# Performance work log

Hardware: AMD Instinct MI355X
Metric: run time of the kernel (lower is better)

Reference implementation:

```python
import jax, jax.numpy as jnp
import numpy as np

B, S, E, H = 4, 2048, 1024, 16
D = E // H


def setup_inputs() -> dict:
    key = jax.random.key(0)
    ks = jax.random.split(key, 6)
    scale = 1.0 / np.sqrt(E).astype(np.float32)
    return {
        "x": jax.random.normal(ks[0], (B, S, E), jnp.float32),
        # positive entries -> cumsum normalizer is well conditioned
        "weight": jax.random.uniform(ks[1], (H, S), jnp.float32, 0.05, 1.0),
        "bias": jax.random.normal(ks[2], (H, S), jnp.float32) * 0.02,
        "inp_w": jax.random.normal(ks[3], (E, E), jnp.float32) * scale,
        "inp_b": jax.random.normal(ks[4], (E,), jnp.float32) * 0.02,
        "out_w": jax.random.normal(ks[5], (E, E), jnp.float32) * scale,
    }


def reference(x, weight, bias, inp_w, inp_b, out_w):
    Bx, Sx, Ex = x.shape
    Hx = weight.shape[0]
    Dx = Ex // Hx
    # input projection (torch Linear: x @ W.T + b)
    x = x @ inp_w.T + inp_b
    # (B,S,E) -> (B,E,S) -> (B,H,D,S)
    xh = x.transpose(0, 2, 1).reshape(Bx, Hx, Dx, Sx)
    # Toeplitz causal matrix per head: M[h,i,j] = weight[h, j-i] if j>=i else 0
    idx = jnp.arange(Sx)
    off = idx[None, :] - idx[:, None]  # (S,S)
    M = jnp.where(off >= 0, weight[:, off], jnp.zeros((), x.dtype))  # (H,S,S)
    # batched matmul over the sequence axis: y[b,h,d,t] = sum_s x[b,h,d,s] M[h,s,t]
    y = jnp.einsum('bhds,hst->bhdt', xh, M)
    # cumulative-sum normalization (do_toep_mean=True)
    norm = jnp.cumsum(weight, axis=-1)  # (H,S)
    y = y / norm[None, :, None, :]
    # per-head, per-position bias
    y = y + bias[None, :, None, :]
    # (B,H,D,S) -> (B,E,S) -> (B,S,E)
    y = y.reshape(Bx, Ex, Sx).transpose(0, 2, 1)
    # output projection (no bias)
    return y @ out_w.T
```

## Files before the change

### kernel.cpp

```cpp
#include <hip/hip_runtime.h>

typedef unsigned short u16;
typedef __attribute__((ext_vector_type(4))) float f32x4;
typedef __attribute__((ext_vector_type(8))) __bf16 bf16x8;

__device__ __forceinline__ u16 f2bf(float f) {
  unsigned u = __builtin_bit_cast(unsigned, f);
  u = u + 0x7fffu + ((u >> 16) & 1u);
  return (u16)(u >> 16);
}

__device__ __forceinline__ void load_lds16(const void* g, void* l) {
  __builtin_amdgcn_global_load_lds((__attribute__((address_space(1))) void*)g,
                                   (__attribute__((address_space(3))) void*)l,
                                   16, 0, 0);
}

__device__ __forceinline__ f32x4 MF(bf16x8 a, bf16x8 b, f32x4 c) {
  return __builtin_amdgcn_mfma_f32_16x16x32_bf16(a, b, c, 0, 0, 0);
}

__global__ __launch_bounds__(256) void prep_all(const float* __restrict__ x,
                                                const float* __restrict__ inp_w,
                                                const float* __restrict__ out_w,
                                                const float* __restrict__ weight,
                                                u16* __restrict__ Xb,
                                                u16* __restrict__ Wb,
                                                u16* __restrict__ OWb,
                                                float* __restrict__ normB,
                                                u16* __restrict__ V) {
  const int bx = blockIdx.x, tid = threadIdx.x;
  if (bx < 10240) {
    const float* src; u16* dst; int i;
    if (bx < 8192)      { src = x;     dst = Xb;  i = bx * 256 + tid; }
    else if (bx < 9216) { src = inp_w; dst = Wb;  i = (bx - 8192) * 256 + tid; }
    else                { src = out_w; dst = OWb; i = (bx - 9216) * 256 + tid; }
    const float4 v = ((const float4*)src)[i];
    ushort4 o;
    o.x = f2bf(v.x); o.y = f2bf(v.y); o.z = f2bf(v.z); o.w = f2bf(v.w);
    ((ushort4*)dst)[i] = o;
    return;
  }
  if (bx < 10256) {
    const int h = bx - 10240;
    __shared__ float ts[256];
    float v[8];
    const float* src = weight + h * 2048 + tid * 8;
    float s = 0.f;
#pragma unroll
    for (int j = 0; j < 8; ++j) v[j] = src[j];
#pragma unroll
    for (int j = 0; j < 8; ++j) { s += v[j]; v[j] = s; }
    ts[tid] = s;
    __syncthreads();
    float xx = s;
#pragma unroll
    for (int d = 1; d < 256; d <<= 1) {
      float y = (tid >= d) ? ts[tid - d] : 0.f;
      __syncthreads();
      xx += y;
      ts[tid] = xx;
      __syncthreads();
    }
    const float excl = xx - s;
    float* dst = normB + h * 2048 + tid * 8;
#pragma unroll
    for (int j = 0; j < 8; ++j) dst[j] = excl + v[j];
    return;
  }
  {
    const int bb = bx - 10256;
    const int h = bb & 15, tb = bb >> 4;
    __shared__ u16 wl[2048];
#pragma unroll
    for (int j = 0; j < 8; ++j) wl[tid * 8 + j] = f2bf(weight[h * 2048 + tid * 8 + j]);
    __syncthreads();
#pragma unroll
    for (int i = 0; i < 8; ++i) {
      const int cid = i * 256 + tid;
      const int row = cid >> 4, c = cid & 15;
      const int t = tb * 128 + row;
      const int j0 = c * 8;
      unsigned v[8];
#pragma unroll
      for (int jj = 0; jj < 8; ++jj) {
        const int j = j0 + jj;
        v[jj] = (t >= j) ? (unsigned)wl[t - j] : 0u;
      }
      uint4 o;
      o.x = v[0] | (v[1] << 16); o.y = v[2] | (v[3] << 16);
      o.z = v[4] | (v[5] << 16); o.w = v[6] | (v[7] << 16);
      *(uint4*)(V + ((size_t)(h * 2048 + t)) * 128 + j0) = o;
    }
  }
}

template <bool BIAS, bool F32OUT, int DEC>
__global__ __launch_bounds__(256) void gemm_nt4(const u16* __restrict__ A,
                                                const u16* __restrict__ B,
                                                void* __restrict__ C,
                                                const float* __restrict__ bias,
                                                int K, int lda, int ldb, int ldc) {
  __shared__ __align__(16) u16 As[2][128 * 64];
  __shared__ __align__(16) u16 Bs[2][128 * 64];
  const int tid = threadIdx.x;
  const int lane = tid & 63, wv = tid >> 6;
  const int wm = wv >> 1, wn = wv & 1;
  const int l15 = lane & 15, g = lane >> 4;

  const int flat = (int)blockIdx.x;
  int m0, n0;
  if (DEC == 0) {
    const int xcd = flat & 7, i = flat >> 3;
    m0 = (i & 7) * 128;
    n0 = ((xcd << 3) + (i >> 3)) * 128;
  } else {
    const int sw = (flat & 7) * 64 + (flat >> 3);
    m0 = (sw >> 3) * 128;
    n0 = (sw & 7) * 128;
  }

  const int NT = K >> 6;

  auto stage = [&](int t, int bi) {
    const int kt = t << 6;
#pragma unroll
    for (int i = 0; i < 4; ++i) {
      const int c = i * 256 + tid;
      const int row = c >> 3, cc = c & 7;
      load_lds16(A + (size_t)(m0 + row) * lda + kt + ((cc ^ (row & 7)) << 3),
                 &As[bi][i * 2048 + wv * 512]);
    }
#pragma unroll
    for (int i = 0; i < 4; ++i) {
      const int c = i * 256 + tid;
      const int row = c >> 3, cc = c & 7;
      load_lds16(B + (size_t)(n0 + row) * ldb + kt + ((cc ^ (row & 7)) << 3),
                 &Bs[bi][i * 2048 + wv * 512]);
    }
  };

  f32x4 acc[4][4] = {};
  stage(0, 0);
  __syncthreads();
  int cur = 0;
  for (int t = 0; t < NT; ++t) {
    if (t + 1 < NT) stage(t + 1, cur ^ 1);
#pragma unroll
    for (int kh = 0; kh < 2; ++kh) {
      bf16x8 af[4], bf[4];
#pragma unroll
      for (int mf = 0; mf < 4; ++mf) {
        const int row = wm * 64 + mf * 16 + l15;
        af[mf] = *(const bf16x8*)(&As[cur][row * 64 + ((((kh << 2) + g) ^ (row & 7)) << 3)]);
      }
#pragma unroll
      for (int nf = 0; nf < 4; ++nf) {
        const int row = wn * 64 + nf * 16 + l15;
        bf[nf] = *(const bf16x8*)(&Bs[cur][row * 64 + ((((kh << 2) + g) ^ (row & 7)) << 3)]);
      }
      __builtin_amdgcn_s_setprio(1);
#pragma unroll
      for (int mf = 0; mf < 4; ++mf)
#pragma unroll
        for (int nf = 0; nf < 4; ++nf)
          acc[mf][nf] = MF(af[mf], bf[nf], acc[mf][nf]);
      __builtin_amdgcn_s_setprio(0);
    }
    __syncthreads();
    cur ^= 1;
  }

#pragma unroll
  for (int mf = 0; mf < 4; ++mf) {
#pragma unroll
    for (int r = 0; r < 4; ++r) {
      const int row = m0 + wm * 64 + mf * 16 + g * 4 + r;
      const float bb = BIAS ? bias[row] : 0.f;
#pragma unroll
      for (int nf = 0; nf < 4; ++nf) {
        const int col = n0 + wn * 64 + nf * 16 + l15;
        const float v = acc[mf][nf][r] + bb;
        if (F32OUT)
          ((float*)C)[(size_t)row * ldc + col] = v;
        else
          ((u16*)C)[(size_t)row * ldc + col] = f2bf(v);
      }
    }
  }
}

__global__ __launch_bounds__(256) void toep_conv(const u16* __restrict__ X1t,
                                                 const u16* __restrict__ V,
                                                 const float* __restrict__ normB,
                                                 const float* __restrict__ biasB,
                                                 u16* __restrict__ Y2b) {
  __shared__ __align__(16) u16 As[3][128 * 64];
  __shared__ __align__(16) u16 Xs[3][64 * 64];
  const int tid = threadIdx.x;
  const int lane = tid & 63, wv = tid >> 6;
  const int l15 = lane & 15, g = lane >> 4;

  const int x = (int)blockIdx.x;
  const int h = (x & 7) + 8 * ((x >> 3) & 1);
  const int pb = x >> 4;
  const int pair = pb & 7, b = pb >> 3;

  const u16* Vh = V + (size_t)h * 2048 * 128;
  const u16* Xrow = X1t + (size_t)h * 64 * 8192 + b * 2048;

#pragma unroll 1
  for (int ti = 0; ti < 2; ++ti) {
    const int tt = ti ? pair : 15 - pair;
    const int t0 = tt * 128;
    const int Q = (tt + 1) * 2;
    f32x4 acc[2][4] = {};

    auto stage = [&](int q, int bufi) {
      const int st = q >> 1, k = q & 1;
      const u16* Ab = Vh + (size_t)(tt - st) * 128 * 128 + k * 64;
#pragma unroll
      for (int i = 0; i < 4; ++i) {
        const int c = i * 256 + tid;
        const int row = c >> 3, cc = c & 7;
        load_lds16(Ab + row * 128 + ((cc ^ (row & 7)) * 8),
                   &As[bufi][i * 2048 + wv * 512]);
      }
      const int s0 = st * 128 + k * 64;
#pragma unroll
      for (int i = 0; i < 2; ++i) {
        const int c = i * 256 + tid;
        const int row = c >> 3, cc = c & 7;
        load_lds16(Xrow + (size_t)row * 8192 + s0 + ((cc ^ (row & 7)) * 8),
                   &Xs[bufi][i * 2048 + wv * 512]);
      }
    };

    stage(0, 0);
    if (Q > 1) stage(1, 1);
    asm volatile("s_waitcnt vmcnt(6)" ::: "memory");
    __builtin_amdgcn_sched_barrier(0);
    __builtin_amdgcn_s_barrier();
    asm volatile("" ::: "memory");

    int cur = 0;
    for (int q = 0; q < Q; ++q) {
      if (q + 2 < Q) stage(q + 2, (q + 2) % 3);
#pragma unroll
      for (int ks = 0; ks < 2; ++ks) {
        bf16x8 af[2];
#pragma unroll
        for (int tf = 0; tf < 2; ++tf) {
          const int row = wv * 32 + tf * 16 + l15;
          af[tf] = *(const bf16x8*)(&As[cur][row * 64 + (((ks * 4 + g) ^ (row & 7)) * 8)]);
        }
#pragma unroll
        for (int nf = 0; nf < 4; ++nf) {
          const int row = nf * 16 + l15;
          const bf16x8 bv = *(const bf16x8*)(&Xs[cur][row * 64 + (((ks * 4 + g) ^ (row & 7)) * 8)]);
#pragma unroll
          for (int tf = 0; tf < 2; ++tf)
            acc[tf][nf] = MF(af[tf], bv, acc[tf][nf]);
        }
      }
      if (q + 2 < Q)      asm volatile("s_waitcnt vmcnt(6)" ::: "memory");
      else if (q + 1 < Q) asm volatile("s_waitcnt vmcnt(0)" ::: "memory");
      __builtin_amdgcn_sched_barrier(0);
      __builtin_amdgcn_s_barrier();
      asm volatile("" ::: "memory");
      cur = (cur == 2) ? 0 : cur + 1;
    }

#pragma unroll
    for (int tf = 0; tf < 2; ++tf) {
#pragma unroll
      for (int r = 0; r < 4; ++r) {
        const int t = t0 + wv * 32 + tf * 16 + g * 4 + r;
        const float inv = 1.0f / normB[h * 2048 + t];
        const float bb = biasB[h * 2048 + t];
#pragma unroll
        for (int nf = 0; nf < 4; ++nf) {
          const int d = nf * 16 + l15;
          Y2b[(size_t)(b * 2048 + t) * 1024 + h * 64 + d] = f2bf(acc[tf][nf][r] * inv + bb);
        }
      }
    }
  }
}

extern "C" void kernel_launch(void* const* d_in, const int* in_sizes, int n_in,
                              void* d_out, int out_size, void* d_ws, size_t ws_size,
                              hipStream_t stream) {
  (void)in_sizes; (void)n_in; (void)out_size; (void)ws_size;
  const float* x      = (const float*)d_in[0];
  const float* weight = (const float*)d_in[1];
  const float* biasB  = (const float*)d_in[2];
  const float* inp_w  = (const float*)d_in[3];
  const float* inp_b  = (const float*)d_in[4];
  const float* out_w  = (const float*)d_in[5];

  char* ws = (char*)d_ws;
  u16* Xb    = (u16*)(ws + 0);
  u16* X1t   = (u16*)(ws + (size_t)(16u << 20));
  u16* Y2b   = (u16*)(ws + (size_t)(32u << 20));
  u16* Wb    = (u16*)(ws + (size_t)(48u << 20));
  u16* OWb   = (u16*)(ws + (size_t)(50u << 20));
  float* normB = (float*)(ws + (size_t)(53u << 20));
  u16* Vt    = (u16*)(ws + (size_t)(56u << 20));

  prep_all<<<10512, 256, 0, stream>>>(x, inp_w, out_w, weight, Xb, Wb, OWb, normB, Vt);

  gemm_nt4<true, false, 0><<<512, 256, 0, stream>>>(
      Wb, Xb, (void*)X1t, inp_b, 1024, 1024, 1024, 8192);

  toep_conv<<<512, 256, 0, stream>>>(X1t, Vt, normB, biasB, Y2b);

  gemm_nt4<false, true, 1><<<512, 256, 0, stream>>>(
      Y2b, OWb, d_out, nullptr, 1024, 1024, 1024, 1024);
}
```

Measured before the change: 97.51 us.

## Share Toeplitz tile across two batches per block, double-buffer instead of triple

Each block of the Toeplitz convolution kernel now handles one output time tile for two batch elements at once, so each loaded Toeplitz (V) tile feeds twice as many MFMAs. The old scheme paired a short and a long time tile within one block. The new one maps short/long tiles across blocks through the v bit. The LDS pipeline drops from triple buffering with explicit vmcnt waits to double buffering with __syncthreads, and s_setprio is raised around the MFMA section. This doubles accumulator registers, may lose load balance, and may expose more memory latency than the deeper pipeline did.

```diff
diff --git a/kernel.cpp b/kernel.cpp
--- a/kernel.cpp
+++ b/kernel.cpp
@@ -195,93 +195,94 @@
                                                  const float* __restrict__ normB,
                                                  const float* __restrict__ biasB,
                                                  u16* __restrict__ Y2b) {
-  __shared__ __align__(16) u16 As[3][128 * 64];
-  __shared__ __align__(16) u16 Xs[3][64 * 64];
+  __shared__ __align__(16) u16 As[2][128 * 64];
+  __shared__ __align__(16) u16 Xs[2][2][64 * 64];
   const int tid = threadIdx.x;
   const int lane = tid & 63, wv = tid >> 6;
   const int l15 = lane & 15, g = lane >> 4;
 
   const int x = (int)blockIdx.x;
   const int h = (x & 7) + 8 * ((x >> 3) & 1);
-  const int pb = x >> 4;
-  const int pair = pb & 7, b = pb >> 3;
+  const int u = (x >> 4) & 15;
+  const int v = (x >> 8) & 1;
+  const int tt = v ? 15 - u : u;
+  const int t0 = tt * 128;
+  const int Q = (tt + 1) * 2;
 
   const u16* Vh = V + (size_t)h * 2048 * 128;
-  const u16* Xrow = X1t + (size_t)h * 64 * 8192 + b * 2048;
-
-#pragma unroll 1
-  for (int ti = 0; ti < 2; ++ti) {
-    const int tt = ti ? pair : 15 - pair;
-    const int t0 = tt * 128;
-    const int Q = (tt + 1) * 2;
-    f32x4 acc[2][4] = {};
-
-    auto stage = [&](int q, int bufi) {
-      const int st = q >> 1, k = q & 1;
-      const u16* Ab = Vh + (size_t)(tt - st) * 128 * 128 + k * 64;
-#pragma unroll
-      for (int i = 0; i < 4; ++i) {
-        const int c = i * 256 + tid;
-        const int row = c >> 3, cc = c & 7;
-        load_lds16(Ab + row * 128 + ((cc ^ (row & 7)) * 8),
-                   &As[bufi][i * 2048 + wv * 512]);
-      }
-      const int s0 = st * 128 + k * 64;
-#pragma unroll
-      for (int i = 0; i < 2; ++i) {
-        const int c = i * 256 + tid;
-        const int row = c >> 3, cc = c & 7;
-        load_lds16(Xrow + (size_t)row * 8192 + s0 + ((cc ^ (row & 7)) * 8),
-                   &Xs[bufi][i * 2048 + wv * 512]);
-      }
-    };
-
-    stage(0, 0);
-    if (Q > 1) stage(1, 1);
-    asm volatile("s_waitcnt vmcnt(6)" ::: "memory");
-    __builtin_amdgcn_sched_barrier(0);
-    __builtin_amdgcn_s_barrier();
-    asm volatile("" ::: "memory");
-
-    int cur = 0;
-    for (int q = 0; q < Q; ++q) {
-      if (q + 2 < Q) stage(q + 2, (q + 2) % 3);
-#pragma unroll
-      for (int ks = 0; ks < 2; ++ks) {
-        bf16x8 af[2];
-#pragma unroll
-        for (int tf = 0; tf < 2; ++tf) {
-          const int row = wv * 32 + tf * 16 + l15;
-          af[tf] = *(const bf16x8*)(&As[cur][row * 64 + (((ks * 4 + g) ^ (row & 7)) * 8)]);
+  const u16* Xrow0 = X1t + (size_t)h * 64 * 8192 + (2 * v + 0) * 2048;
+  const u16* Xrow1 = X1t + (size_t)h * 64 * 8192 + (2 * v + 1) * 2048;
+
+  auto stage = [&](int q, int bi) {
+    const int st = q >> 1, k = q & 1;
+    const u16* Ab = Vh + (size_t)(tt - st) * 128 * 128 + k * 64;
+#pragma unroll
+    for (int i = 0; i < 4; ++i) {
+      const int c = i * 256 + tid;
+      const int row = c >> 3, cc = c & 7;
+      load_lds16(Ab + row * 128 + ((cc ^ (row & 7)) << 3),
+                 &As[bi][i * 2048 + wv * 512]);
+    }
+    const int s0 = st * 128 + k * 64;
+    const int srow = tid >> 3, scc = tid & 7;
+    const size_t xoff = (size_t)srow * 8192 + s0 + ((scc ^ (srow & 7)) << 3);
+#pragma unroll
+    for (int i = 0; i < 2; ++i) {
+      const int c = i * 256 + tid;
+      const int row = c >> 3, cc = c & 7;
+      const size_t off = (size_t)row * 8192 + s0 + ((cc ^ (row & 7)) << 3);
+      load_lds16(Xrow0 + off, &Xs[bi][0][i * 2048 + wv * 512]);
+      load_lds16(Xrow1 + off, &Xs[bi][1][i * 2048 + wv * 512]);
+    }
+    (void)xoff;
+  };
+
+  f32x4 acc[2][2][4] = {};
+  stage(0, 0);
+  __syncthreads();
+  int cur = 0;
+  for (int q = 0; q < Q; ++q) {
+    if (q + 1 < Q) stage(q + 1, cur ^ 1);
+#pragma unroll
+    for (int ks = 0; ks < 2; ++ks) {
+      bf16x8 af[2];
+#pragma unroll
+      for (int tf = 0; tf < 2; ++tf) {
+        const int row = wv * 32 + tf * 16 + l15;
+        af[tf] = *(const bf16x8*)(&As[cur][row * 64 + ((((ks << 2) + g) ^ (row & 7)) << 3)]);
+      }
+      __builtin_amdgcn_s_setprio(1);
+#pragma unroll
+      for (int bb = 0; bb < 2; ++bb) {
+#pragma unroll
+        for (int nf = 0; nf < 4; ++nf) {
+          const int drow = nf * 16 + l15;
+          const bf16x8 bv = *(const bf16x8*)(&Xs[cur][bb][drow * 64 + ((((ks << 2) + g) ^ (drow & 7)) << 3)]);
+#pragma unroll
+          for (int tf = 0; tf < 2; ++tf)
+            acc[bb][tf][nf] = MF(af[tf], bv, acc[bb][tf][nf]);
         }
-#pragma unroll
-        for (int nf = 0; nf < 4; ++nf) {
-          const int row = nf * 16 + l15;
-          const bf16x8 bv = *(const bf16x8*)(&Xs[cur][row * 64 + (((ks * 4 + g) ^ (row & 7)) * 8)]);
-#pragma unroll
-          for (int tf = 0; tf < 2; ++tf)
-            acc[tf][nf] = MF(af[tf], bv, acc[tf][nf]);
-        }
-      }
-      if (q + 2 < Q)      asm volatile("s_waitcnt vmcnt(6)" ::: "memory");
-      else if (q + 1 < Q) asm volatile("s_waitcnt vmcnt(0)" ::: "memory");
-      __builtin_amdgcn_sched_barrier(0);
-      __builtin_amdgcn_s_barrier();
-      asm volatile("" ::: "memory");
-      cur = (cur == 2) ? 0 : cur + 1;
-    }
-
+      }
+      __builtin_amdgcn_s_setprio(0);
+    }
+    __syncthreads();
+    cur ^= 1;
+  }
+
+#pragma unroll
+  for (int bb = 0; bb < 2; ++bb) {
+    const int b = 2 * v + bb;
 #pragma unroll
     for (int tf = 0; tf < 2; ++tf) {
 #pragma unroll
       for (int r = 0; r < 4; ++r) {
         const int t = t0 + wv * 32 + tf * 16 + g * 4 + r;
         const float inv = 1.0f / normB[h * 2048 + t];
-        const float bb = biasB[h * 2048 + t];
+        const float bbv = biasB[h * 2048 + t];
 #pragma unroll
         for (int nf = 0; nf < 4; ++nf) {
           const int d = nf * 16 + l15;
-          Y2b[(size_t)(b * 2048 + t) * 1024 + h * 64 + d] = f2bf(acc[tf][nf][r] * inv + bb);
+          Y2b[(size_t)(b * 2048 + t) * 1024 + h * 64 + d] = f2bf(acc[bb][tf][nf][r] * inv + bbv);
         }
       }
     }
```

After: 108.2 us. +11.0%, slower.
